# Optimization experiments

Measured on AMD Instinct MI355X. Metric: run time of the kernel, lower is better.

Reference implementation:

```python
import math
import jax, jax.numpy as jnp
import numpy as np

SR = 22050
FRAME_SIZE = 1025
MAX_FILTER_SIZE = 20
B, T = 16, 2048


def _build_transform_matrix(frame_size=FRAME_SIZE, sr=SR, max_filter_size=MAX_FILTER_SIZE):
    max_freq = sr / 2
    freq = np.linspace(0, max_freq, num=frame_size, endpoint=True)
    mel = 2595 * np.log10(1 + freq / 700)
    min_mel, max_mel = mel[0], mel[-1]
    raw = (mel - min_mel) / (max_mel - min_mel) * (max_filter_size - 1) + 1
    mtx = np.zeros((frame_size, frame_size), dtype=np.float32)
    for i in range(frame_size):
        fs = math.floor(raw[i]) // 2 * 2 + 1
        start, end = i - fs // 2, i + fs // 2 + 1
        start, end = max(0, start), min(end, frame_size)
        mtx[i, start:end] = 1.0 / (end - start)
    return jnp.asarray(mtx)


def setup_inputs() -> dict:
    key = jax.random.key(0)
    k1, k2 = jax.random.split(key)
    model_output = jax.random.normal(k1, (B, FRAME_SIZE, T), dtype=jnp.float32)
    target = jax.random.normal(k2, (B, FRAME_SIZE, T), dtype=jnp.float32)
    transform_matrix = _build_transform_matrix()
    return {"model_output": model_output, "target": target, "transform_matrix": transform_matrix}


def reference(model_output, target, transform_matrix):
    # db_to_amp(x)**2 == (10**(x/20))**2 == 10**(x/10)
    mo = jnp.power(10.0, model_output / 10.0)
    tg = jnp.power(10.0, target / 10.0)
    diff = mo - tg  # [B, F, T]
    # mel-scale variable-width mean filter applied as dense matmul, per original
    filtered = jnp.einsum('ij,bjt->bit', transform_matrix, diff)
    return jnp.mean(filtered ** 2)
```

## Files before the change

kernel.cpp:

```cpp
#include <hip/hip_runtime.h>


#define F 1025
#define TT 2048
#define BB 16
#define NSEG 12
#define SEG 86
#define RING 24
#define TPB 256
#define TCH 512
#define NTB (TT / TCH)
#define NBLK (BB * NTB * NSEG)
#define CHUNK 4

__global__ __launch_bounds__(256) void band_kernel(const float* __restrict__ mtx,
                                                   int* __restrict__ bs,
                                                   int* __restrict__ be,
                                                   float* __restrict__ binv) {
    int row  = blockIdx.x * 4 + (threadIdx.x >> 6);
    int lane = threadIdx.x & 63;
    if (row >= F) return;
    const float* r = mtx + (size_t)row * F;
    int first = -1, last = -1;
    for (int c = 0; c < (F + 63) / 64; ++c) {
        int j = c * 64 + lane;
        float v = (j < F) ? r[j] : 0.0f;
        unsigned long long m = __ballot(v != 0.0f);
        if (m) {
            if (first < 0) first = c * 64 + (__ffsll((unsigned long long)m) - 1);
            last = c * 64 + (63 - __clzll((long long)m));
        }
    }
    if (lane == 0) {
        bs[row]   = first;
        be[row]   = last + 1;
        binv[row] = r[first];
    }
}

__global__ __launch_bounds__(TPB) void mel_mse_kernel(const float* __restrict__ mo,
                                                      const float* __restrict__ tg,
                                                      const int* __restrict__ bs,
                                                      const int* __restrict__ be,
                                                      const float* __restrict__ binv,
                                                      double* __restrict__ partial) {
    const int tid = threadIdx.x;
    const int blk = blockIdx.x;
    const int s  = blk % NSEG;
    const int r_ = blk / NSEG;
    const int tb = r_ % NTB;
    const int b  = r_ / NTB;

    const int i0 = s * SEG;
    const int i1 = (i0 + SEG < F) ? (i0 + SEG) : F;
    const int nrows = i1 - i0;

    __shared__ float2 ring[RING * TPB];
    __shared__ int    be_l[SEG];
    __shared__ int    bs_l[SEG];
    __shared__ float  binv_l[SEG];

    if (tid < nrows) {
        be_l[tid]   = be[i0 + tid];
        bs_l[tid]   = bs[i0 + tid];
        binv_l[tid] = binv[i0 + tid];
    }
    __syncthreads();

    const int jstart = bs_l[0];
    const int jend   = be_l[nrows - 1];

    const int ct = tb * TPB + tid;
    const float2* __restrict__ moP = (const float2*)(mo + (size_t)b * F * TT) + ct;
    const float2* __restrict__ tgP = (const float2*)(tg + (size_t)b * F * TT) + ct;
    const size_t rs = TT / 2;

    const float C = 0.33219281f;

    float2 A0[CHUNK], G0[CHUNK], A1[CHUNK], G1[CHUNK], A2[CHUNK], G2[CHUNK];

#define LOADC(Ad, Gd, jbase)                                        \
    _Pragma("unroll")                                               \
    for (int r = 0; r < CHUNK; ++r) {                               \
        int jr = (jbase) + r;                                       \
        jr = (jr < jend) ? jr : (jend - 1);                         \
        Ad[r] = moP[(size_t)jr * rs];                               \
        Gd[r] = tgP[(size_t)jr * rs];                               \
    }

    LOADC(A0, G0, jstart)
    LOADC(A1, G1, jstart + CHUNK)

    float wx = 0.0f, wy = 0.0f, acc = 0.0f;
    int i = 0, cs = jstart, wp = 0, rp = 0;

    for (int j = jstart; j < jend; j += CHUNK) {
        LOADC(A2, G2, j + 2 * CHUNK)
        #pragma unroll
        for (int r = 0; r < CHUNK; ++r) {
            if (j + r < jend) {
                const float dx = __builtin_amdgcn_exp2f(A0[r].x * C)
                               - __builtin_amdgcn_exp2f(G0[r].x * C);
                const float dy = __builtin_amdgcn_exp2f(A0[r].y * C)
                               - __builtin_amdgcn_exp2f(G0[r].y * C);
                float2 dv; dv.x = dx; dv.y = dy;
                ring[wp + tid] = dv;
                wp += TPB; if (wp == RING * TPB) wp = 0;
                wx += dx; wy += dy;
                while (i < nrows && be_l[i] <= j + r + 1) {
                    const int si = bs_l[i];
                    while (cs < si) {
                        const float2 o = ring[rp + tid];
                        rp += TPB; if (rp == RING * TPB) rp = 0;
                        wx -= o.x; wy -= o.y;
                        ++cs;
                    }
                    const float inv = binv_l[i];
                    const float fx = wx * inv, fy = wy * inv;
                    acc = fmaf(fx, fx, fmaf(fy, fy, acc));
                    ++i;
                }
            }
        }
        #pragma unroll
        for (int r = 0; r < CHUNK; ++r) {
            A0[r] = A1[r]; G0[r] = G1[r];
            A1[r] = A2[r]; G1[r] = G2[r];
        }
    }
#undef LOADC

    #pragma unroll
    for (int off = 32; off > 0; off >>= 1)
        acc += __shfl_down(acc, off, 64);

    __shared__ double wred[4];
    const int wid = tid >> 6, lane = tid & 63;
    if (lane == 0) wred[wid] = (double)acc;
    __syncthreads();
    if (tid == 0)
        partial[blk] = wred[0] + wred[1] + wred[2] + wred[3];
}

__global__ __launch_bounds__(256) void final_kernel(const double* __restrict__ partial,
                                                    float* __restrict__ out) {
    const int tid = threadIdx.x;
    double s = 0.0;
    for (int k = tid; k < NBLK; k += 256) s += partial[k];
    #pragma unroll
    for (int off = 32; off > 0; off >>= 1)
        s += __shfl_down(s, off, 64);
    __shared__ double wred[4];
    const int wid = tid >> 6, lane = tid & 63;
    if (lane == 0) wred[wid] = s;
    __syncthreads();
    if (tid == 0) {
        double tot = wred[0] + wred[1] + wred[2] + wred[3];
        out[0] = (float)(tot / ((double)BB * (double)F * (double)TT));
    }
}

extern "C" void kernel_launch(void* const* d_in, const int* in_sizes, int n_in,
                              void* d_out, int out_size, void* d_ws, size_t ws_size,
                              hipStream_t stream) {
    const float* mo  = (const float*)d_in[0];
    const float* tg  = (const float*)d_in[1];
    const float* mtx = (const float*)d_in[2];

    char* ws = (char*)d_ws;
    int*    bs      = (int*)(ws);
    int*    be      = (int*)(ws + 8192);
    float*  binv    = (float*)(ws + 16384);
    double* partial = (double*)(ws + 24576);

    band_kernel<<<(F + 3) / 4, 256, 0, stream>>>(mtx, bs, be, binv);
    mel_mse_kernel<<<NBLK, TPB, 0, stream>>>(mo, tg, bs, be, binv, partial);
    final_kernel<<<1, 256, 0, stream>>>(partial, (float*)d_out);
}
```

Baseline: 69.89 us.

## Process one column per thread with scalar loads and a smaller ring buffer

Each thread now handles a single time column with scalar float loads instead of two columns with float2 loads. This doubles the number of time blocks and grid size and halves the ring buffer's shared memory. The kernel also gains a minimum of 6 blocks per SM in its launch bounds, aimed at higher occupancy. In exchange, global accesses are narrower and the per-thread overhead of the banding loop and the band-boundary data is repeated across twice as many blocks.

```diff
diff --git a/kernel.cpp b/kernel.cpp
--- a/kernel.cpp
+++ b/kernel.cpp
@@ -8,8 +8,7 @@
 #define SEG 86
 #define RING 24
 #define TPB 256
-#define TCH 512
-#define NTB (TT / TCH)
+#define NTB (TT / TPB)
 #define NBLK (BB * NTB * NSEG)
 #define CHUNK 4
 
@@ -38,12 +37,12 @@
     }
 }
 
-__global__ __launch_bounds__(TPB) void mel_mse_kernel(const float* __restrict__ mo,
-                                                      const float* __restrict__ tg,
-                                                      const int* __restrict__ bs,
-                                                      const int* __restrict__ be,
-                                                      const float* __restrict__ binv,
-                                                      double* __restrict__ partial) {
+__global__ __launch_bounds__(TPB, 6) void mel_mse_kernel(const float* __restrict__ mo,
+                                                         const float* __restrict__ tg,
+                                                         const int* __restrict__ bs,
+                                                         const int* __restrict__ be,
+                                                         const float* __restrict__ binv,
+                                                         double* __restrict__ partial) {
     const int tid = threadIdx.x;
     const int blk = blockIdx.x;
     const int s  = blk % NSEG;
@@ -55,10 +54,10 @@
     const int i1 = (i0 + SEG < F) ? (i0 + SEG) : F;
     const int nrows = i1 - i0;
 
-    __shared__ float2 ring[RING * TPB];
-    __shared__ int    be_l[SEG];
-    __shared__ int    bs_l[SEG];
-    __shared__ float  binv_l[SEG];
+    __shared__ float ring[RING * TPB];
+    __shared__ int   be_l[SEG];
+    __shared__ int   bs_l[SEG];
+    __shared__ float binv_l[SEG];
 
     if (tid < nrows) {
         be_l[tid]   = be[i0 + tid];
@@ -70,14 +69,14 @@
     const int jstart = bs_l[0];
     const int jend   = be_l[nrows - 1];
 
-    const int ct = tb * TPB + tid;
-    const float2* __restrict__ moP = (const float2*)(mo + (size_t)b * F * TT) + ct;
-    const float2* __restrict__ tgP = (const float2*)(tg + (size_t)b * F * TT) + ct;
-    const size_t rs = TT / 2;
+    const int t = tb * TPB + tid;
+    const float* __restrict__ moP = mo + (size_t)b * F * TT + t;
+    const float* __restrict__ tgP = tg + (size_t)b * F * TT + t;
+    const size_t rs = TT;
 
     const float C = 0.33219281f;
 
-    float2 A0[CHUNK], G0[CHUNK], A1[CHUNK], G1[CHUNK], A2[CHUNK], G2[CHUNK];
+    float A0[CHUNK], G0[CHUNK], A1[CHUNK], G1[CHUNK], A2[CHUNK], G2[CHUNK];
 
 #define LOADC(Ad, Gd, jbase)                                        \
     _Pragma("unroll")                                               \
@@ -91,7 +90,7 @@
     LOADC(A0, G0, jstart)
     LOADC(A1, G1, jstart + CHUNK)
 
-    float wx = 0.0f, wy = 0.0f, acc = 0.0f;
+    float wsum = 0.0f, acc = 0.0f;
     int i = 0, cs = jstart, wp = 0, rp = 0;
 
     for (int j = jstart; j < jend; j += CHUNK) {
@@ -99,25 +98,20 @@
         #pragma unroll
         for (int r = 0; r < CHUNK; ++r) {
             if (j + r < jend) {
-                const float dx = __builtin_amdgcn_exp2f(A0[r].x * C)
-                               - __builtin_amdgcn_exp2f(G0[r].x * C);
-                const float dy = __builtin_amdgcn_exp2f(A0[r].y * C)
-                               - __builtin_amdgcn_exp2f(G0[r].y * C);
-                float2 dv; dv.x = dx; dv.y = dy;
-                ring[wp + tid] = dv;
+                const float d = __builtin_amdgcn_exp2f(A0[r] * C)
+                              - __builtin_amdgcn_exp2f(G0[r] * C);
+                ring[wp + tid] = d;
                 wp += TPB; if (wp == RING * TPB) wp = 0;
-                wx += dx; wy += dy;
+                wsum += d;
                 while (i < nrows && be_l[i] <= j + r + 1) {
                     const int si = bs_l[i];
                     while (cs < si) {
-                        const float2 o = ring[rp + tid];
+                        wsum -= ring[rp + tid];
                         rp += TPB; if (rp == RING * TPB) rp = 0;
-                        wx -= o.x; wy -= o.y;
                         ++cs;
                     }
-                    const float inv = binv_l[i];
-                    const float fx = wx * inv, fy = wy * inv;
-                    acc = fmaf(fx, fx, fmaf(fy, fy, acc));
+                    const float f = wsum * binv_l[i];
+                    acc = fmaf(f, f, acc);
                     ++i;
                 }
             }
```

New measurement: 71.54 us. 2.4% more time.
